# Performance work log

Hardware: AMD Instinct MI355X
Metric: run time of the kernel (lower is better)

Reference implementation:

```python
import jax, jax.numpy as jnp
import numpy as np

N = 50000
IN_C, HID, OUT_C = 128, 64, 40


def setup_inputs() -> dict:
    key = jax.random.key(0)
    ks = jax.random.split(key, 10)
    x = jax.random.normal(ks[0], (N, IN_C), dtype=jnp.float32)
    edge_index = jax.random.randint(ks[1], (2, 1600000), 0, N, dtype=jnp.int64)
    edge_attr = jax.random.uniform(ks[2], (1600000,), dtype=jnp.float32)
    def lin(k, fan_in, fan_out):
        bound = 1.0 / np.sqrt(fan_in)
        return jax.random.uniform(k, (fan_in, fan_out), jnp.float32, -bound, bound)
    W1 = lin(ks[3], IN_C, HID); b1 = jnp.zeros((HID,), jnp.float32)
    W2 = lin(ks[4], HID, HID); b2 = jnp.zeros((HID,), jnp.float32)
    W3 = lin(ks[5], HID, OUT_C); b3 = jnp.zeros((OUT_C,), jnp.float32)
    return {"x": x, "edge_index": edge_index, "edge_attr": edge_attr,
            "W1": W1, "b1": b1, "W2": W2, "b2": b2, "W3": W3, "b3": b3}


def _gcn_conv(x, src, dst, norm, W, b):
    # h = x W ; out[i] = sum_{(j->i)} norm_e * h[j] ; + bias
    h = x @ W
    msg = norm[:, None] * h[src]          # [E+N, F_out] gathered messages
    out = jax.ops.segment_sum(msg, dst, num_segments=N)
    return out + b


def reference(x, edge_index, edge_attr, W1, b1, W2, b2, W3, b3):
    # GCN normalization with self-loops (fill_value=1), cached across layers.
    loops = jnp.arange(N, dtype=edge_index.dtype)
    src = jnp.concatenate([edge_index[0], loops])
    dst = jnp.concatenate([edge_index[1], loops])
    w = jnp.concatenate([edge_attr, jnp.ones((N,), edge_attr.dtype)])
    deg = jnp.zeros((N,), x.dtype).at[dst].add(w)
    dinv = jnp.where(deg > 0, jax.lax.rsqrt(deg), 0.0)
    norm = dinv[src] * w * dinv[dst]

    h = jax.nn.relu(_gcn_conv(x, src, dst, norm, W1, b1))   # dropout: eval no-op
    h = jax.nn.relu(_gcn_conv(h, src, dst, norm, W2, b2))
    h = jax.nn.relu(_gcn_conv(h, src, dst, norm, W3, b3))
    return jax.nn.log_softmax(h, axis=-1)
```

## Files before the change

kernel.cpp:

```cpp
#include <hip/hip_runtime.h>
#include <math.h>

#define N_NODES 50000
#define E_EDGES 1600000
#define IN_C    128
#define HID     64
#define OUT_C   40

#define BSH     9
#define BNODES  512
#define NB      98
#define CAP     20480
#define PBS     28160
#define TILE    4096
#define P1T     512
#define NPB     16

typedef unsigned int uint;
typedef unsigned short ushort;

__device__ inline float b2f(ushort h) { return __uint_as_float(((uint)h) << 16); }
__device__ inline ushort f2b(float f) {
    uint u = __float_as_uint(f);
    u += 0x7FFFu + ((u >> 16) & 1u);
    return (ushort)(u >> 16);
}
#define BLO(u) __uint_as_float((u) << 16)
#define BHI(u) __uint_as_float((u) & 0xFFFF0000u)
#define FMA8(A, B, v, ww) do { \
    (A).x += (ww) * BLO((v).x); (A).y += (ww) * BHI((v).x); \
    (A).z += (ww) * BLO((v).y); (A).w += (ww) * BHI((v).y); \
    (B).x += (ww) * BLO((v).z); (B).y += (ww) * BHI((v).z); \
    (B).z += (ww) * BLO((v).w); (B).w += (ww) * BHI((v).w); } while (0)

__global__ __launch_bounds__(P1T) void k_bin(const int* __restrict__ ei,
                                             const float* __restrict__ w,
                                             int* __restrict__ bcursor,
                                             uint2* __restrict__ tmp) {
    __shared__ uint2 stage[TILE];
    __shared__ unsigned char sbuck[TILE];
    __shared__ int hist[NB], startb[NB], cursor[NB], baseg[NB];
    __shared__ int sc[128];
    const int tid = threadIdx.x;
    const int e0  = blockIdx.x * TILE;
    const int n   = min(TILE, E_EDGES - e0);

    for (int i = tid; i < NB; i += P1T) hist[i] = 0;
    __syncthreads();

    for (int i = tid; i < n; i += P1T) {
        int d = ei[E_EDGES + e0 + i];
        atomicAdd(&hist[d >> BSH], 1);
    }
    __syncthreads();

    if (tid < 128) sc[tid] = (tid < NB) ? hist[tid] : 0;
    __syncthreads();
    for (int off = 1; off < 128; off <<= 1) {
        int x = 0;
        if (tid < 128 && tid >= off) x = sc[tid - off];
        __syncthreads();
        if (tid < 128) sc[tid] += x;
        __syncthreads();
    }
    if (tid < NB) {
        int st = sc[tid] - hist[tid];
        startb[tid] = st;
        cursor[tid] = st;
        baseg[tid]  = atomicAdd(&bcursor[tid], hist[tid]);
    }
    __syncthreads();

    for (int i = tid; i < n; i += P1T) {
        int   s  = ei[e0 + i];
        int   d  = ei[E_EDGES + e0 + i];
        float wv = w[e0 + i];
        int   b  = d >> BSH;
        int pos = atomicAdd(&cursor[b], 1);
        stage[pos] = make_uint2(((uint)(d & (BNODES - 1)) << 16) | (uint)s,
                                __float_as_uint(wv));
        sbuck[pos] = (unsigned char)b;
    }
    __syncthreads();

    for (int i = tid; i < n; i += P1T) {
        int b = sbuck[i];
        int gpos = baseg[b] + (i - startb[b]);
        tmp[(size_t)b * CAP + gpos] = stage[i];
    }
}

__global__ __launch_bounds__(BNODES) void k_build(const int* __restrict__ bcursor,
                                                  const uint2* __restrict__ tmp,
                                                  uint* __restrict__ rowinfo,
                                                  float* __restrict__ dinv,
                                                  uint* __restrict__ csr) {
    __shared__ int   hist[BNODES];
    __shared__ float wsum[BNODES];
    __shared__ int   sc[BNODES];
    __shared__ int   cur[BNODES];
    const int tid = threadIdx.x;
    const int b   = blockIdx.x;
    const int cnt = bcursor[b];
    const uint2* tb = tmp + (size_t)b * CAP;

    hist[tid] = 0; wsum[tid] = 0.0f;
    __syncthreads();
    for (int i = tid; i < cnt; i += BNODES) {
        uint2 u = tb[i];
        int dl = u.x >> 16;
        atomicAdd(&hist[dl], 1);
        atomicAdd(&wsum[dl], __uint_as_float(u.y));
    }
    __syncthreads();

    const int deg  = hist[tid];
    const int pdeg = (deg + 15) & ~15;
    sc[tid] = pdeg;
    __syncthreads();
    for (int off = 1; off < BNODES; off <<= 1) {
        int x = (tid >= off) ? sc[tid - off] : 0;
        __syncthreads();
        sc[tid] += x;
        __syncthreads();
    }
    const int base = b * PBS + (sc[tid] - pdeg);
    const int node = (b << BSH) + tid;
    if (node < N_NODES) {
        rowinfo[node] = ((uint)(pdeg >> 4) << 24) | (uint)base;
        dinv[node]    = rsqrtf(1.0f + wsum[tid]);
    }
    cur[tid] = base;
    __syncthreads();

    for (int i = tid; i < cnt; i += BNODES) {
        uint2 u = tb[i];
        int dl = u.x >> 16;
        int pos = atomicAdd(&cur[dl], 1);
        csr[pos] = ((uint)f2b(__uint_as_float(u.y)) << 16) | (u.x & 0xFFFFu);
    }
    for (int i = deg; i < pdeg; ++i) csr[base + i] = 0u;
}

__global__ __launch_bounds__(256) void k_gemm1(const float* __restrict__ x,
                                               const float* __restrict__ W,
                                               const float* __restrict__ dinv,
                                               ushort* __restrict__ g) {
    __shared__ float sW[IN_C * HID];
    __shared__ float sx[NPB * IN_C];
    const int tid = threadIdx.x;
    const size_t base = (size_t)blockIdx.x * NPB;

    for (int i = tid; i < (IN_C * HID) / 4; i += 256)
        ((float4*)sW)[i] = ((const float4*)W)[i];
    for (int i = tid; i < (NPB * IN_C) / 4; i += 256)
        ((float4*)sx)[i] = ((const float4*)(x + base * IN_C))[i];
    __syncthreads();

    const int wv = tid >> 6, f = tid & 63;
    for (int nn = 0; nn < 4; ++nn) {
        const int nl = wv * 4 + nn;
        const float* row = &sx[nl * IN_C];
        float acc = 0.0f;
#pragma unroll 8
        for (int k = 0; k < IN_C; k += 4) {
            float4 a = *(const float4*)&row[k];
            acc += a.x * sW[(k + 0) * HID + f] + a.y * sW[(k + 1) * HID + f]
                 + a.z * sW[(k + 2) * HID + f] + a.w * sW[(k + 3) * HID + f];
        }
        const size_t node = base + nl;
        g[node * HID + f] = f2b(dinv[node] * acc);
    }
}

template <int F_OUT>
__global__ __launch_bounds__(256) void k_agg_gemm(const uint* __restrict__ rowinfo,
                                                  const uint* __restrict__ csr,
                                                  const ushort* __restrict__ g,
                                                  const float* __restrict__ dinv,
                                                  const float* __restrict__ bias,
                                                  const float* __restrict__ W,
                                                  ushort* __restrict__ g_next) {
    __shared__ float sW[HID * F_OUT];
    __shared__ float s_act[4][HID];
    const int tid = threadIdx.x;
    for (int i = tid; i < HID * F_OUT; i += 256) sW[i] = W[i];

    const int wv = tid >> 6, lane = tid & 63;
    const int node  = blockIdx.x * 4 + wv;
    const int grp   = lane >> 3;
    const int sub   = lane & 7;
    const int dslot = lane & 15;
    const uint ri  = rowinfo[node];
    const int  n16 = (int)(ri >> 24);
    const float dv = dinv[node];
    const ushort* gs = g + (size_t)sub * 8;

    float4 accA = {0.f, 0.f, 0.f, 0.f}, accB = accA;
    if (grp == 0) {
        uint4 v = ((const uint4*)(g + (size_t)node * HID))[sub];
        accA.x = BLO(v.x); accA.y = BHI(v.x); accA.z = BLO(v.y); accA.w = BHI(v.y);
        accB.x = BLO(v.z); accB.y = BHI(v.z); accB.z = BLO(v.w); accB.w = BHI(v.w);
    }

    if (n16 > 0) {
        const uint* rp = csr + (ri & 0xFFFFFFu) + dslot;
        uint d1 = rp[0];
        uint sA = __shfl(d1, grp), sB = __shfl(d1, 8 + grp);
        float wA = BHI(sA), wB = BHI(sB);
        uint4 A = *(const uint4*)(gs + (size_t)(sA & 0xFFFFu) * HID);
        uint4 B = *(const uint4*)(gs + (size_t)(sB & 0xFFFFu) * HID);
        d1 = rp[16];
        for (int blk = 1; blk < n16; ++blk) {
            uint d2 = rp[(blk + 1) << 4];
            uint sA2 = __shfl(d1, grp), sB2 = __shfl(d1, 8 + grp);
            float wA2 = BHI(sA2), wB2 = BHI(sB2);
            uint4 A2 = *(const uint4*)(gs + (size_t)(sA2 & 0xFFFFu) * HID);
            uint4 B2 = *(const uint4*)(gs + (size_t)(sB2 & 0xFFFFu) * HID);
            FMA8(accA, accB, A, wA);
            FMA8(accA, accB, B, wB);
            d1 = d2; A = A2; B = B2; wA = wA2; wB = wB2;
        }
        FMA8(accA, accB, A, wA);
        FMA8(accA, accB, B, wB);
    }
#pragma unroll
    for (int m = 8; m <= 32; m <<= 1) {
        accA.x += __shfl_xor(accA.x, m); accA.y += __shfl_xor(accA.y, m);
        accA.z += __shfl_xor(accA.z, m); accA.w += __shfl_xor(accA.w, m);
        accB.x += __shfl_xor(accB.x, m); accB.y += __shfl_xor(accB.y, m);
        accB.z += __shfl_xor(accB.z, m); accB.w += __shfl_xor(accB.w, m);
    }
    if (grp == 0) {
        float4 bA = ((const float4*)bias)[2 * sub];
        float4 bB = ((const float4*)bias)[2 * sub + 1];
        float4 rA, rB;
        rA.x = fmaxf(dv * accA.x + bA.x, 0.f); rA.y = fmaxf(dv * accA.y + bA.y, 0.f);
        rA.z = fmaxf(dv * accA.z + bA.z, 0.f); rA.w = fmaxf(dv * accA.w + bA.w, 0.f);
        rB.x = fmaxf(dv * accB.x + bB.x, 0.f); rB.y = fmaxf(dv * accB.y + bB.y, 0.f);
        rB.z = fmaxf(dv * accB.z + bB.z, 0.f); rB.w = fmaxf(dv * accB.w + bB.w, 0.f);
        ((float4*)&s_act[wv][0])[2 * sub]     = rA;
        ((float4*)&s_act[wv][0])[2 * sub + 1] = rB;
    }
    __syncthreads();
    if (lane < F_OUT) {
        float dot = 0.0f;
#pragma unroll 4
        for (int k = 0; k < HID; k += 4) {
            float4 a = *(const float4*)&s_act[wv][k];
            dot += a.x * sW[(k + 0) * F_OUT + lane] + a.y * sW[(k + 1) * F_OUT + lane]
                 + a.z * sW[(k + 2) * F_OUT + lane] + a.w * sW[(k + 3) * F_OUT + lane];
        }
        g_next[(size_t)node * F_OUT + lane] = f2b(dinv[node] * dot);
    }
}

__global__ __launch_bounds__(256) void k_final_agg(const uint* __restrict__ rowinfo,
                                                   const uint* __restrict__ csr,
                                                   const ushort* __restrict__ g,
                                                   const float* __restrict__ dinv,
                                                   const float* __restrict__ bias,
                                                   float* __restrict__ out) {
    const int tid = threadIdx.x;
    const int wv = tid >> 6, lane = tid & 63;
    const int node  = blockIdx.x * 4 + wv;
    const int grp   = lane >> 3;
    const int sub   = lane & 7;
    const int dslot = lane & 15;
    const bool live = sub < (OUT_C / 8);
    const uint ri  = rowinfo[node];
    const int  n16 = (int)(ri >> 24);
    const float dv = dinv[node];
    const ushort* gs = g + (size_t)sub * 8;

    float4 accA = {0.f, 0.f, 0.f, 0.f}, accB = accA;
    if (grp == 0 && live) {
        uint4 v = ((const uint4*)(g + (size_t)node * OUT_C))[sub];
        accA.x = BLO(v.x); accA.y = BHI(v.x); accA.z = BLO(v.y); accA.w = BHI(v.y);
        accB.x = BLO(v.z); accB.y = BHI(v.z); accB.z = BLO(v.w); accB.w = BHI(v.w);
    }

    if (n16 > 0) {
        const uint* rp = csr + (ri & 0xFFFFFFu) + dslot;
        uint d1 = rp[0];
        uint sA = __shfl(d1, grp), sB = __shfl(d1, 8 + grp);
        float wA = BHI(sA), wB = BHI(sB);
        uint4 A = *(const uint4*)(gs + (size_t)(sA & 0xFFFFu) * OUT_C);
        uint4 B = *(const uint4*)(gs + (size_t)(sB & 0xFFFFu) * OUT_C);
        d1 = rp[16];
        for (int blk = 1; blk < n16; ++blk) {
            uint d2 = rp[(blk + 1) << 4];
            uint sA2 = __shfl(d1, grp), sB2 = __shfl(d1, 8 + grp);
            float wA2 = BHI(sA2), wB2 = BHI(sB2);
            uint4 A2 = *(const uint4*)(gs + (size_t)(sA2 & 0xFFFFu) * OUT_C);
            uint4 B2 = *(const uint4*)(gs + (size_t)(sB2 & 0xFFFFu) * OUT_C);
            FMA8(accA, accB, A, wA);
            FMA8(accA, accB, B, wB);
            d1 = d2; A = A2; B = B2; wA = wA2; wB = wB2;
        }
        FMA8(accA, accB, A, wA);
        FMA8(accA, accB, B, wB);
    }
#pragma unroll
    for (int m = 8; m <= 32; m <<= 1) {
        accA.x += __shfl_xor(accA.x, m); accA.y += __shfl_xor(accA.y, m);
        accA.z += __shfl_xor(accA.z, m); accA.w += __shfl_xor(accA.w, m);
        accB.x += __shfl_xor(accB.x, m); accB.y += __shfl_xor(accB.y, m);
        accB.z += __shfl_xor(accB.z, m); accB.w += __shfl_xor(accB.w, m);
    }

    const bool own = (grp == 0) && live;
    float4 vA = {0.f, 0.f, 0.f, 0.f}, vB = vA;
    if (own) {
        float4 bA = ((const float4*)bias)[2 * sub];
        float4 bB = ((const float4*)bias)[2 * sub + 1];
        vA.x = fmaxf(dv * accA.x + bA.x, 0.f); vA.y = fmaxf(dv * accA.y + bA.y, 0.f);
        vA.z = fmaxf(dv * accA.z + bA.z, 0.f); vA.w = fmaxf(dv * accA.w + bA.w, 0.f);
        vB.x = fmaxf(dv * accB.x + bB.x, 0.f); vB.y = fmaxf(dv * accB.y + bB.y, 0.f);
        vB.z = fmaxf(dv * accB.z + bB.z, 0.f); vB.w = fmaxf(dv * accB.w + bB.w, 0.f);
    }
    float mx = own ? fmaxf(fmaxf(fmaxf(vA.x, vA.y), fmaxf(vA.z, vA.w)),
                           fmaxf(fmaxf(vB.x, vB.y), fmaxf(vB.z, vB.w))) : -INFINITY;
#pragma unroll
    for (int off = 1; off < 8; off <<= 1) mx = fmaxf(mx, __shfl_xor(mx, off));
    float se = own ? (expf(vA.x - mx) + expf(vA.y - mx) + expf(vA.z - mx) + expf(vA.w - mx)
                    + expf(vB.x - mx) + expf(vB.y - mx) + expf(vB.z - mx) + expf(vB.w - mx)) : 0.f;
#pragma unroll
    for (int off = 1; off < 8; off <<= 1) se += __shfl_xor(se, off);
    if (own) {
        float lg = mx + logf(se);
        float4 oA, oB;
        oA.x = vA.x - lg; oA.y = vA.y - lg; oA.z = vA.z - lg; oA.w = vA.w - lg;
        oB.x = vB.x - lg; oB.y = vB.y - lg; oB.z = vB.z - lg; oB.w = vB.w - lg;
        ((float4*)(out + (size_t)node * OUT_C))[2 * sub]     = oA;
        ((float4*)(out + (size_t)node * OUT_C))[2 * sub + 1] = oB;
    }
}

extern "C" void kernel_launch(void* const* d_in, const int* in_sizes, int n_in,
                              void* d_out, int out_size, void* d_ws, size_t ws_size,
                              hipStream_t stream) {
    const float* x  = (const float*)d_in[0];
    const int*   ei = (const int*)d_in[1];
    const float* w  = (const float*)d_in[2];
    const float* W1 = (const float*)d_in[3];
    const float* b1 = (const float*)d_in[4];
    const float* W2 = (const float*)d_in[5];
    const float* b2 = (const float*)d_in[6];
    const float* W3 = (const float*)d_in[7];
    const float* b3 = (const float*)d_in[8];
    float* out = (float*)d_out;

    char* ws = (char*)d_ws;
    size_t off = 0;
    auto carve = [&](size_t bytes) {
        char* p = ws + off;
        off += (bytes + 255) & ~(size_t)255;
        return p;
    };
    int*   bcursor = (int*)carve(NB * sizeof(int));
    uint*  rowinfo = (uint*)carve(N_NODES * sizeof(uint));
    float* dinv    = (float*)carve(N_NODES * sizeof(float));
    uint*  csr     = (uint*)carve(((size_t)NB * PBS + 64) * sizeof(uint));
    uint2* tmp     = (uint2*)carve((size_t)NB * CAP * sizeof(uint2));
    ushort* g1 = (ushort*)tmp;
    ushort* g2 = g1 + (size_t)N_NODES * HID;
    ushort* g3 = g1;
    (void)ws_size;

    const int nbBin = (E_EDGES + TILE - 1) / TILE;
    const int nbN4  = N_NODES / 4;
    const int nbG1  = N_NODES / NPB;

    hipMemsetAsync(bcursor, 0, NB * sizeof(int), stream);
    k_bin<<<nbBin, P1T, 0, stream>>>(ei, w, bcursor, tmp);
    k_build<<<NB, BNODES, 0, stream>>>(bcursor, tmp, rowinfo, dinv, csr);

    k_gemm1<<<nbG1, 256, 0, stream>>>(x, W1, dinv, g1);
    k_agg_gemm<HID><<<nbN4, 256, 0, stream>>>(rowinfo, csr, g1, dinv, b1, W2, g2);
    k_agg_gemm<OUT_C><<<nbN4, 256, 0, stream>>>(rowinfo, csr, g2, dinv, b2, W3, g3);
    k_final_agg<<<nbN4, 256, 0, stream>>>(rowinfo, csr, g3, dinv, b3, out);
}
```

Before: 242.6 us.

## Use feature-per-lane gather with readlane broadcast in aggregation kernels

Rewrites the neighbor aggregation in the fused agg+GEMM and final aggregation kernels. Before, eight groups of eight lanes each loaded 16-byte uint4 chunks for different edges and were combined with a cross-group shuffle reduction. Now each lane owns one feature column, every edge descriptor is broadcast via readlane, and each lane loads 2-byte bf16 values for 16 edges per block. This removes the shuffle reductions and simplifies the log-softmax, but issues many more, narrower gather loads, and lanes 40-63 sit idle in the 40-channel kernels.

```diff
diff --git a/kernel.cpp b/kernel.cpp
--- a/kernel.cpp
+++ b/kernel.cpp
@@ -25,13 +25,6 @@
     u += 0x7FFFu + ((u >> 16) & 1u);
     return (ushort)(u >> 16);
 }
-#define BLO(u) __uint_as_float((u) << 16)
-#define BHI(u) __uint_as_float((u) & 0xFFFF0000u)
-#define FMA8(A, B, v, ww) do { \
-    (A).x += (ww) * BLO((v).x); (A).y += (ww) * BHI((v).x); \
-    (A).z += (ww) * BLO((v).y); (A).w += (ww) * BHI((v).y); \
-    (B).x += (ww) * BLO((v).z); (B).y += (ww) * BHI((v).z); \
-    (B).z += (ww) * BLO((v).w); (B).w += (ww) * BHI((v).w); } while (0)
 
 __global__ __launch_bounds__(P1T) void k_bin(const int* __restrict__ ei,
                                              const float* __restrict__ w,
@@ -187,61 +180,37 @@
     for (int i = tid; i < HID * F_OUT; i += 256) sW[i] = W[i];
 
     const int wv = tid >> 6, lane = tid & 63;
-    const int node  = blockIdx.x * 4 + wv;
-    const int grp   = lane >> 3;
-    const int sub   = lane & 7;
-    const int dslot = lane & 15;
+    const int node = blockIdx.x * 4 + wv;
     const uint ri  = rowinfo[node];
     const int  n16 = (int)(ri >> 24);
     const float dv = dinv[node];
-    const ushort* gs = g + (size_t)sub * 8;
-
-    float4 accA = {0.f, 0.f, 0.f, 0.f}, accB = accA;
-    if (grp == 0) {
-        uint4 v = ((const uint4*)(g + (size_t)node * HID))[sub];
-        accA.x = BLO(v.x); accA.y = BHI(v.x); accA.z = BLO(v.y); accA.w = BHI(v.y);
-        accB.x = BLO(v.z); accB.y = BHI(v.z); accB.z = BLO(v.w); accB.w = BHI(v.w);
-    }
-
-    if (n16 > 0) {
-        const uint* rp = csr + (ri & 0xFFFFFFu) + dslot;
-        uint d1 = rp[0];
-        uint sA = __shfl(d1, grp), sB = __shfl(d1, 8 + grp);
-        float wA = BHI(sA), wB = BHI(sB);
-        uint4 A = *(const uint4*)(gs + (size_t)(sA & 0xFFFFu) * HID);
-        uint4 B = *(const uint4*)(gs + (size_t)(sB & 0xFFFFu) * HID);
-        d1 = rp[16];
-        for (int blk = 1; blk < n16; ++blk) {
-            uint d2 = rp[(blk + 1) << 4];
-            uint sA2 = __shfl(d1, grp), sB2 = __shfl(d1, 8 + grp);
-            float wA2 = BHI(sA2), wB2 = BHI(sB2);
-            uint4 A2 = *(const uint4*)(gs + (size_t)(sA2 & 0xFFFFu) * HID);
-            uint4 B2 = *(const uint4*)(gs + (size_t)(sB2 & 0xFFFFu) * HID);
-            FMA8(accA, accB, A, wA);
-            FMA8(accA, accB, B, wB);
-            d1 = d2; A = A2; B = B2; wA = wA2; wB = wB2;
-        }
-        FMA8(accA, accB, A, wA);
-        FMA8(accA, accB, B, wB);
-    }
-#pragma unroll
-    for (int m = 8; m <= 32; m <<= 1) {
-        accA.x += __shfl_xor(accA.x, m); accA.y += __shfl_xor(accA.y, m);
-        accA.z += __shfl_xor(accA.z, m); accA.w += __shfl_xor(accA.w, m);
-        accB.x += __shfl_xor(accB.x, m); accB.y += __shfl_xor(accB.y, m);
-        accB.z += __shfl_xor(accB.z, m); accB.w += __shfl_xor(accB.w, m);
-    }
-    if (grp == 0) {
-        float4 bA = ((const float4*)bias)[2 * sub];
-        float4 bB = ((const float4*)bias)[2 * sub + 1];
-        float4 rA, rB;
-        rA.x = fmaxf(dv * accA.x + bA.x, 0.f); rA.y = fmaxf(dv * accA.y + bA.y, 0.f);
-        rA.z = fmaxf(dv * accA.z + bA.z, 0.f); rA.w = fmaxf(dv * accA.w + bA.w, 0.f);
-        rB.x = fmaxf(dv * accB.x + bB.x, 0.f); rB.y = fmaxf(dv * accB.y + bB.y, 0.f);
-        rB.z = fmaxf(dv * accB.z + bB.z, 0.f); rB.w = fmaxf(dv * accB.w + bB.w, 0.f);
-        ((float4*)&s_act[wv][0])[2 * sub]     = rA;
-        ((float4*)&s_act[wv][0])[2 * sub + 1] = rB;
-    }
+
+    float acc0 = b2f(g[(size_t)node * HID + lane]);
+    float acc1 = 0.0f;
+
+    const uint* rp = csr + (ri & 0xFFFFFFu);
+    uint d = rp[lane & 15];
+    for (int blk = 0; blk < n16; ++blk) {
+        uint dn = rp[((blk + 1) << 4) + (lane & 15)];
+        ushort uv[16];
+        uint   sw[16];
+#pragma unroll
+        for (int j = 0; j < 16; ++j) {
+            uint dj = (uint)__builtin_amdgcn_readlane((int)d, j);
+            sw[j] = dj & 0xFFFF0000u;
+            uv[j] = g[(size_t)(dj & 0xFFFFu) * HID + lane];
+        }
+#pragma unroll
+        for (int j = 0; j < 16; ++j) {
+            float f = b2f(uv[j]);
+            if (j & 1) acc1 += __uint_as_float(sw[j]) * f;
+            else       acc0 += __uint_as_float(sw[j]) * f;
+        }
+        d = dn;
+    }
+    float acc = acc0 + acc1;
+
+    s_act[wv][lane] = fmaxf(dv * acc + bias[lane], 0.0f);
     __syncthreads();
     if (lane < F_OUT) {
         float dot = 0.0f;
@@ -263,78 +232,47 @@
                                                    float* __restrict__ out) {
     const int tid = threadIdx.x;
     const int wv = tid >> 6, lane = tid & 63;
-    const int node  = blockIdx.x * 4 + wv;
-    const int grp   = lane >> 3;
-    const int sub   = lane & 7;
-    const int dslot = lane & 15;
-    const bool live = sub < (OUT_C / 8);
+    const int node = blockIdx.x * 4 + wv;
+    const bool live = lane < OUT_C;
     const uint ri  = rowinfo[node];
     const int  n16 = (int)(ri >> 24);
     const float dv = dinv[node];
-    const ushort* gs = g + (size_t)sub * 8;
-
-    float4 accA = {0.f, 0.f, 0.f, 0.f}, accB = accA;
-    if (grp == 0 && live) {
-        uint4 v = ((const uint4*)(g + (size_t)node * OUT_C))[sub];
-        accA.x = BLO(v.x); accA.y = BHI(v.x); accA.z = BLO(v.y); accA.w = BHI(v.y);
-        accB.x = BLO(v.z); accB.y = BHI(v.z); accB.z = BLO(v.w); accB.w = BHI(v.w);
-    }
-
-    if (n16 > 0) {
-        const uint* rp = csr + (ri & 0xFFFFFFu) + dslot;
-        uint d1 = rp[0];
-        uint sA = __shfl(d1, grp), sB = __shfl(d1, 8 + grp);
-        float wA = BHI(sA), wB = BHI(sB);
-        uint4 A = *(const uint4*)(gs + (size_t)(sA & 0xFFFFu) * OUT_C);
-        uint4 B = *(const uint4*)(gs + (size_t)(sB & 0xFFFFu) * OUT_C);
-        d1 = rp[16];
-        for (int blk = 1; blk < n16; ++blk) {
-            uint d2 = rp[(blk + 1) << 4];
-            uint sA2 = __shfl(d1, grp), sB2 = __shfl(d1, 8 + grp);
-            float wA2 = BHI(sA2), wB2 = BHI(sB2);
-            uint4 A2 = *(const uint4*)(gs + (size_t)(sA2 & 0xFFFFu) * OUT_C);
-            uint4 B2 = *(const uint4*)(gs + (size_t)(sB2 & 0xFFFFu) * OUT_C);
-            FMA8(accA, accB, A, wA);
-            FMA8(accA, accB, B, wB);
-            d1 = d2; A = A2; B = B2; wA = wA2; wB = wB2;
-        }
-        FMA8(accA, accB, A, wA);
-        FMA8(accA, accB, B, wB);
-    }
-#pragma unroll
-    for (int m = 8; m <= 32; m <<= 1) {
-        accA.x += __shfl_xor(accA.x, m); accA.y += __shfl_xor(accA.y, m);
-        accA.z += __shfl_xor(accA.z, m); accA.w += __shfl_xor(accA.w, m);
-        accB.x += __shfl_xor(accB.x, m); accB.y += __shfl_xor(accB.y, m);
-        accB.z += __shfl_xor(accB.z, m); accB.w += __shfl_xor(accB.w, m);
-    }
-
-    const bool own = (grp == 0) && live;
-    float4 vA = {0.f, 0.f, 0.f, 0.f}, vB = vA;
-    if (own) {
-        float4 bA = ((const float4*)bias)[2 * sub];
-        float4 bB = ((const float4*)bias)[2 * sub + 1];
-        vA.x = fmaxf(dv * accA.x + bA.x, 0.f); vA.y = fmaxf(dv * accA.y + bA.y, 0.f);
-        vA.z = fmaxf(dv * accA.z + bA.z, 0.f); vA.w = fmaxf(dv * accA.w + bA.w, 0.f);
-        vB.x = fmaxf(dv * accB.x + bB.x, 0.f); vB.y = fmaxf(dv * accB.y + bB.y, 0.f);
-        vB.z = fmaxf(dv * accB.z + bB.z, 0.f); vB.w = fmaxf(dv * accB.w + bB.w, 0.f);
-    }
-    float mx = own ? fmaxf(fmaxf(fmaxf(vA.x, vA.y), fmaxf(vA.z, vA.w)),
-                           fmaxf(fmaxf(vB.x, vB.y), fmaxf(vB.z, vB.w))) : -INFINITY;
-#pragma unroll
-    for (int off = 1; off < 8; off <<= 1) mx = fmaxf(mx, __shfl_xor(mx, off));
-    float se = own ? (expf(vA.x - mx) + expf(vA.y - mx) + expf(vA.z - mx) + expf(vA.w - mx)
-                    + expf(vB.x - mx) + expf(vB.y - mx) + expf(vB.z - mx) + expf(vB.w - mx)) : 0.f;
-#pragma unroll
-    for (int off = 1; off < 8; off <<= 1) se += __shfl_xor(se, off);
-    if (own) {
-        float lg = mx + logf(se);
-        float4 oA, oB;
-        oA.x = vA.x - lg; oA.y = vA.y - lg; oA.z = vA.z - lg; oA.w = vA.w - lg;
-        oB.x = vB.x - lg; oB.y = vB.y - lg; oB.z = vB.z - lg; oB.w = vB.w - lg;
-        ((float4*)(out + (size_t)node * OUT_C))[2 * sub]     = oA;
-        ((float4*)(out + (size_t)node * OUT_C))[2 * sub + 1] = oB;
-    }
+
+    float acc0 = live ? b2f(g[(size_t)node * OUT_C + lane]) : 0.0f;
+    float acc1 = 0.0f;
+
+    const uint* rp = csr + (ri & 0xFFFFFFu);
+    uint d = rp[lane & 15];
+    for (int blk = 0; blk < n16; ++blk) {
+        uint dn = rp[((blk + 1) << 4) + (lane & 15)];
+        ushort uv[16];
+        uint   sw[16];
+#pragma unroll
+        for (int j = 0; j < 16; ++j) {
+            uint dj = (uint)__builtin_amdgcn_readlane((int)d, j);
+            sw[j] = dj & 0xFFFF0000u;
+            uv[j] = g[(size_t)(dj & 0xFFFFu) * OUT_C + lane];
+        }
+#pragma unroll
+        for (int j = 0; j < 16; ++j) {
+            float f = b2f(uv[j]);
+            if (j & 1) acc1 += __uint_as_float(sw[j]) * f;
+            else       acc0 += __uint_as_float(sw[j]) * f;
+        }
+        d = dn;
+    }
+    float acc = acc0 + acc1;
+
+    float bl = live ? bias[lane] : 0.0f;
+    float v  = live ? fmaxf(dv * acc + bl, 0.0f) : -INFINITY;
+    float mx = v;
+#pragma unroll
+    for (int off = 32; off > 0; off >>= 1) mx = fmaxf(mx, __shfl_xor(mx, off));
+    float ex = live ? expf(v - mx) : 0.0f;
+    float se = ex;
+#pragma unroll
+    for (int off = 32; off > 0; off >>= 1) se += __shfl_xor(se, off);
+    if (live) out[(size_t)node * OUT_C + lane] = v - mx - logf(se);
 }
 
 extern "C" void kernel_launch(void* const* d_in, const int* in_sizes, int n_in,
@@ -362,7 +300,7 @@
     uint*  rowinfo = (uint*)carve(N_NODES * sizeof(uint));
     float* dinv    = (float*)carve(N_NODES * sizeof(float));
     uint*  csr     = (uint*)carve(((size_t)NB * PBS + 64) * sizeof(uint));
-    uint2* tmp     = (uint2*)carve((size_t)NB * CAP * sizeof(uint2));
+    uint2* tmp     = (uint2*)carve((size_t)NB * CAP * sizeof(uint2) + 256);
     ushort* g1 = (ushort*)tmp;
     ushort* g2 = g1 + (size_t)N_NODES * HID;
     ushort* g3 = g1;
```

Measured after the change: 240.6 us. No clear change (-0.8%).
